# Performance work log

Measured on AMD Instinct MI355X. Metric: run time of the kernel, lower is better.

The kernel has to match this reference:

```python
import jax, jax.numpy as jnp
import numpy as np

# dims
H = 1024          # hidden_size
E = 2048          # d_inner = 2*H
NH = 32           # nheads = E/64
P = 64            # headdim
N = 128           # d_state
G = 1             # ngroups
K = 4             # d_conv
Q = 128           # SSD chunk length
FF = 4096         # intermediate_size
EPS = 1e-6        # rms_norm_eps
NEPS = 1e-5       # mamba gated-norm eps
CONV_DIM = E + 2 * G * N            # 2304
D_IN = 2 * E + 2 * G * N + NH       # 4384


def rmsnorm(x, w, eps):
    v = jnp.mean(x.astype(jnp.float32) ** 2, axis=-1, keepdims=True)
    return (x.astype(jnp.float32) * jax.lax.rsqrt(v + eps)).astype(x.dtype) * w


def segsum(x):
    # x: [..., T] -> [..., T, T] with out[i,j] = sum_{j<k<=i} x[k], -inf above diag
    T = x.shape[-1]
    cs = jnp.cumsum(x, axis=-1)
    s = cs[..., :, None] - cs[..., None, :]
    mask = jnp.tril(jnp.ones((T, T), dtype=bool))
    return jnp.where(mask, s, -jnp.inf)


def ssd(x, dt, A_log, B, C):
    # x:[b,l,nh,p], dt:[b,l,nh], B,C:[b,l,N] (ngroups=1, shared over heads)
    b, l, nh, p = x.shape
    A = -jnp.exp(A_log)                      # [nh]
    dA = dt * A                              # [b,l,nh]
    xd = x * dt[..., None]                   # discretized input
    c = l // Q
    xd = xd.reshape(b, c, Q, nh, p)
    dAc = dA.reshape(b, c, Q, nh).transpose(0, 3, 1, 2)   # [b,h,c,q]
    Bc = B.reshape(b, c, Q, N)
    Cc = C.reshape(b, c, Q, N)
    A_cs = jnp.cumsum(dAc, axis=-1)                        # [b,h,c,q]
    Lm = jnp.exp(segsum(dAc))                              # [b,h,c,q,q]
    # intra-chunk (diagonal blocks)
    Y_diag = jnp.einsum('bcqn,bcsn,bhcqs,bcshp->bcqhp', Cc, Bc, Lm, xd)
    # per-chunk final states
    decay_states = jnp.exp(A_cs[..., -1:] - A_cs)          # [b,h,c,q]
    states = jnp.einsum('bcqn,bhcq,bcqhp->bchpn', Bc, decay_states, xd)
    # inter-chunk recurrence (initial state = 0)
    A_last = jnp.pad(A_cs[..., -1], ((0, 0), (0, 0), (1, 0)))   # [b,h,c+1]
    decay_chunk = jnp.exp(segsum(A_last))                       # [b,h,c+1,c+1]
    states = jnp.concatenate([jnp.zeros_like(states[:, :1]), states], axis=1)
    new_states = jnp.einsum('bhzc,bchpn->bzhpn', decay_chunk, states)[:, :-1]
    Y_off = jnp.einsum('bcqn,bchpn,bhcq->bcqhp', Cc, new_states, jnp.exp(A_cs))
    return (Y_diag + Y_off).reshape(b, l, nh, p)


def mamba2(h, w_in, w_conv, b_conv, dt_bias, A_log, D, w_mnorm, w_out):
    b, l, _ = h.shape
    zxbcdt = h @ w_in.T                         # [b,l,D_IN]
    z, xBC, dt = jnp.split(zxbcdt, [E, E + CONV_DIM], axis=-1)
    # causal depthwise conv (kernel K) over channels of xBC
    pad = jnp.pad(xBC, ((0, 0), (K - 1, 0), (0, 0)))
    xBC = sum(pad[:, k:k + l, :] * w_conv[:, k] for k in range(K)) + b_conv
    xBC = jax.nn.silu(xBC)
    x, B, C = jnp.split(xBC, [E, E + G * N], axis=-1)
    dt = jax.nn.softplus(dt + dt_bias)          # [b,l,NH]
    xh = x.reshape(b, l, NH, P)
    y = ssd(xh, dt, A_log, B, C)
    y = y + D[None, None, :, None] * xh         # per-head skip
    y = y.reshape(b, l, E)
    y = rmsnorm(y * jax.nn.silu(z), w_mnorm, NEPS)   # gated RMSNorm
    return y @ w_out.T


def setup_inputs() -> dict:
    key = jax.random.key(0)
    ks = jax.random.split(key, 12)
    dt0 = jax.random.uniform(ks[0], (NH,), minval=0.001, maxval=0.1)
    dt_bias = dt0 + jnp.log(-jnp.expm1(-dt0))   # inverse softplus
    return {
        'hidden_states': jax.random.normal(ks[1], (2, 2048, H), dtype=jnp.float32),
        'w_ln1': jnp.ones((H,), jnp.float32),
        'w_in': 0.02 * jax.random.normal(ks[2], (D_IN, H), dtype=jnp.float32),
        'w_conv': 0.1 * jax.random.normal(ks[3], (CONV_DIM, K), dtype=jnp.float32),
        'b_conv': jnp.zeros((CONV_DIM,), jnp.float32),
        'dt_bias': dt_bias,
        'A_log': jnp.log(jax.random.uniform(ks[4], (NH,), minval=1.0, maxval=16.0)),
        'D': jnp.ones((NH,), jnp.float32),
        'w_mnorm': jnp.ones((E,), jnp.float32),
        'w_out': 0.02 * jax.random.normal(ks[5], (H, E), dtype=jnp.float32),
        'w_ln2': jnp.ones((H,), jnp.float32),
        'w_gate': 0.02 * jax.random.normal(ks[6], (FF, H), dtype=jnp.float32),
        'w_up': 0.02 * jax.random.normal(ks[7], (FF, H), dtype=jnp.float32),
        'w_down': 0.02 * jax.random.normal(ks[8], (H, FF), dtype=jnp.float32),
    }


def reference(hidden_states, w_ln1, w_in, w_conv, b_conv, dt_bias, A_log, D,
              w_mnorm, w_out, w_ln2, w_gate, w_up, w_down):
    residual = hidden_states
    h = rmsnorm(hidden_states, w_ln1, EPS)
    h = mamba2(h, w_in, w_conv, b_conv, dt_bias, A_log, D, w_mnorm, w_out)
    hidden = residual + h
    residual = hidden
    h = rmsnorm(hidden, w_ln2, EPS)
    h = (jax.nn.silu(h @ w_gate.T) * (h @ w_up.T)) @ w_down.T
    return residual + h
```

## Files before the change

### kernel.cpp

```cpp
#include <hip/hip_runtime.h>

#define DEV static __device__ __forceinline__

typedef short bf16x8 __attribute__((ext_vector_type(8)));
typedef float floatx4 __attribute__((ext_vector_type(4)));
typedef unsigned short ushort4v __attribute__((ext_vector_type(4)));
typedef unsigned short ushort8v __attribute__((ext_vector_type(8)));

DEV unsigned short f32_bf16(float f) {
  unsigned int u = __builtin_bit_cast(unsigned int, f);
  u = u + 0x7fffu + ((u >> 16) & 1u);
  return (unsigned short)(u >> 16);
}
DEV float bf2f(unsigned short u) {
  unsigned int v = ((unsigned int)u) << 16;
  return __builtin_bit_cast(float, v);
}
DEV float sigmoidf_(float x) { return 1.0f / (1.0f + __expf(-x)); }
DEV float siluf_(float x) { return x * sigmoidf_(x); }

#define GLD_LDS16(g, l)                                                              \
  __builtin_amdgcn_global_load_lds((const __attribute__((address_space(1))) void*)(g), \
                                   (__attribute__((address_space(3))) void*)(l), 16, 0, 0)

template <int MODE>
__global__ __launch_bounds__(256) void gemm128(
    const unsigned short* __restrict__ A, const unsigned short* __restrict__ B,
    void* __restrict__ Cv, const unsigned short* __restrict__ other,
    int K, int lda, int ldb, int ldc, long long bsA, long long bsB, long long bsC) {
  __shared__ unsigned short As[2 * 128 * 32];
  __shared__ unsigned short Bs[2 * 128 * 32];
  A += (long long)blockIdx.z * bsA;
  B += (long long)blockIdx.z * bsB;
  const long long coff = (long long)blockIdx.z * bsC;
  const int tid = threadIdx.x;
  const int w = tid >> 6, lane = tid & 63;

  const int nbx = gridDim.x, nby = gridDim.y;
  const int GM = 4;
  int bid = blockIdx.y * nbx + blockIdx.x;
  int gid = bid / (GM * nbx);
  int rem = bid - gid * (GM * nbx);
  int gsz = min(GM, nby - gid * GM);
  int mtile = gid * GM + rem % gsz;
  int ntile = rem / gsz;
  const int m0 = mtile << 7, n0 = ntile << 7;

  const int srow = lane >> 2;
  const int schunk = ((lane & 3) ^ (srow & 3)) * 8;
  const unsigned short* ag0 = A + (long long)(m0 + w * 32 + srow) * lda + schunk;
  const unsigned short* ag1 = ag0 + (long long)16 * lda;
  const unsigned short* bg0 = B + (long long)(n0 + w * 32 + srow) * ldb + schunk;
  const unsigned short* bg1 = bg0 + (long long)16 * ldb;
  const int s_off = w * 1024 + lane * 8;

#define STAGE128(buf, k0)                              \
  do {                                                 \
    GLD_LDS16(ag0 + (k0), As + (buf) * 4096 + s_off);  \
    GLD_LDS16(ag1 + (k0), As + (buf) * 4096 + s_off + 512); \
    GLD_LDS16(bg0 + (k0), Bs + (buf) * 4096 + s_off);  \
    GLD_LDS16(bg1 + (k0), Bs + (buf) * 4096 + s_off + 512); \
  } while (0)

  const int wr = (w >> 1) << 6, wc = (w & 1) << 6;
  const int fr = lane & 15;
  const int slot = (((lane >> 4) ^ (fr & 3))) << 3;

  floatx4 acc[4][4];
#pragma unroll
  for (int i = 0; i < 4; ++i)
#pragma unroll
    for (int j = 0; j < 4; ++j) acc[i][j] = (floatx4){0.f, 0.f, 0.f, 0.f};

  const int nsteps = K >> 5;
  STAGE128(0, 0);
  if (nsteps > 1) STAGE128(1, 32);

  for (int t = 0; t < nsteps; ++t) {
    if (t < nsteps - 1) {
      asm volatile("s_waitcnt vmcnt(4)" ::: "memory");
    } else {
      asm volatile("s_waitcnt vmcnt(0)" ::: "memory");
    }
    __builtin_amdgcn_s_barrier();
    __builtin_amdgcn_sched_barrier(0);
    const unsigned short* Ab = As + (t & 1) * 4096;
    const unsigned short* Bb = Bs + (t & 1) * 4096;
    bf16x8 af[4], bf_[4];
#pragma unroll
    for (int i = 0; i < 4; ++i)
      af[i] = *(const bf16x8*)(Ab + (wr + i * 16 + fr) * 32 + slot);
#pragma unroll
    for (int j = 0; j < 4; ++j)
      bf_[j] = *(const bf16x8*)(Bb + (wc + j * 16 + fr) * 32 + slot);
#pragma unroll
    for (int i = 0; i < 4; ++i)
#pragma unroll
      for (int j = 0; j < 4; ++j)
        acc[i][j] = __builtin_amdgcn_mfma_f32_16x16x32_bf16(af[i], bf_[j], acc[i][j], 0, 0, 0);
    __builtin_amdgcn_sched_barrier(0);
    __builtin_amdgcn_s_barrier();
    if (t + 2 < nsteps) STAGE128(t & 1, (t + 2) * 32);
  }
#undef STAGE128

  const int r0 = (lane >> 4) << 2;
#pragma unroll
  for (int i = 0; i < 4; ++i) {
#pragma unroll
    for (int j = 0; j < 4; ++j) {
      long long base = (long long)(m0 + wr + i * 16 + r0) * ldc + (n0 + wc + j * 16 + fr);
#pragma unroll
      for (int r = 0; r < 4; ++r) {
        long long idx = coff + base + (long long)r * ldc;
        float v = acc[i][j][r];
        if constexpr (MODE == 0) {
          ((float*)Cv)[idx] = v;
        } else if constexpr (MODE == 1) {
          ((unsigned short*)Cv)[idx] = f32_bf16(v);
        } else {
          ((unsigned short*)Cv)[idx] = f32_bf16(siluf_(v) * bf2f(other[idx]));
        }
      }
    }
  }
}

template <int WM>
__global__ __launch_bounds__(256) void gemm_small_nt(
    const unsigned short* __restrict__ A, const unsigned short* __restrict__ B,
    float* __restrict__ C, int M, int N, int K, int lda, int ldb, int ldc) {
  const int w = threadIdx.x >> 6;
  const int lane = threadIdx.x & 63;
  const int lm = lane & 15;
  const int ko = (lane >> 4) << 3;
  const int bn0 = blockIdx.x << 6;
  const int m_base = blockIdx.y * (WM * 64) + w * (WM * 16);

  const unsigned short* arow[WM];
#pragma unroll
  for (int i = 0; i < WM; ++i) arow[i] = A + (long long)(m_base + i * 16 + lm) * lda + ko;
  int nv = (N - bn0) >> 4;
  nv = nv > 4 ? 4 : nv;
  const unsigned short* brow[4];
#pragma unroll
  for (int j = 0; j < 4; ++j) {
    int nr = bn0 + j * 16 + lm;
    brow[j] = B + (long long)(j < nv ? nr : 0) * ldb + ko;
  }
  floatx4 acc[WM][4];
#pragma unroll
  for (int i = 0; i < WM; ++i)
#pragma unroll
    for (int j = 0; j < 4; ++j) acc[i][j] = (floatx4){0.f, 0.f, 0.f, 0.f};
  for (int k0 = 0; k0 < K; k0 += 32) {
    bf16x8 a[WM];
#pragma unroll
    for (int i = 0; i < WM; ++i) a[i] = *(const bf16x8*)(arow[i] + k0);
#pragma unroll
    for (int j = 0; j < 4; ++j) {
      if (j < nv) {
        bf16x8 b = *(const bf16x8*)(brow[j] + k0);
#pragma unroll
        for (int i = 0; i < WM; ++i)
          acc[i][j] = __builtin_amdgcn_mfma_f32_16x16x32_bf16(a[i], b, acc[i][j], 0, 0, 0);
      }
    }
  }
  const int r0 = (lane >> 4) << 2;
#pragma unroll
  for (int i = 0; i < WM; ++i)
#pragma unroll
    for (int j = 0; j < 4; ++j)
      if (j < nv) {
        int col = bn0 + j * 16 + lm;
        long long base = (long long)(m_base + i * 16 + r0) * ldc + col;
#pragma unroll
        for (int r = 0; r < 4; ++r) C[base + (long long)r * ldc] = acc[i][j][r];
      }
}

__global__ __launch_bounds__(256) void f32_to_bf16_k(const float* __restrict__ src,
                                                     unsigned short* __restrict__ dst,
                                                     long long n4) {
  long long i = (long long)blockIdx.x * 256 + threadIdx.x;
  if (i < n4) {
    float4 v = ((const float4*)src)[i];
    ushort4v o = {f32_bf16(v.x), f32_bf16(v.y), f32_bf16(v.z), f32_bf16(v.w)};
    ((ushort4v*)dst)[i] = o;
  }
}

__global__ __launch_bounds__(256) void zero_out_k(float* __restrict__ o, long long n) {
  long long i = (long long)blockIdx.x * 256 + threadIdx.x;
  if (i < n) o[i] = 0.f;
}

__global__ __launch_bounds__(256) void rmsnorm1024_bf16_k(const float* __restrict__ x,
                                                          const float* __restrict__ w,
                                                          unsigned short* __restrict__ out,
                                                          float eps) {
  long long row = blockIdx.x;
  int t = threadIdx.x;
  float4 v = ((const float4*)(x + row * 1024))[t];
  float ss = v.x * v.x + v.y * v.y + v.z * v.z + v.w * v.w;
  __shared__ float red[4];
#pragma unroll
  for (int o = 32; o > 0; o >>= 1) ss += __shfl_down(ss, o, 64);
  if ((t & 63) == 0) red[t >> 6] = ss;
  __syncthreads();
  float tot = red[0] + red[1] + red[2] + red[3];
  float sc = rsqrtf(tot * (1.0f / 1024.0f) + eps);
  float4 wv = ((const float4*)w)[t];
  ushort4v o = {f32_bf16(v.x * sc * wv.x), f32_bf16(v.y * sc * wv.y),
                f32_bf16(v.z * sc * wv.z), f32_bf16(v.w * sc * wv.w)};
  ((ushort4v*)(out + row * 1024))[t] = o;
}

__global__ __launch_bounds__(256) void add_rmsnorm_k(const float* __restrict__ hs,
                                                     const float* __restrict__ parts,
                                                     long long pstride, int np,
                                                     const float* __restrict__ w,
                                                     float* __restrict__ mh,
                                                     unsigned short* __restrict__ h2, float eps) {
  long long row = blockIdx.x;
  int t = threadIdx.x;
  float4 v = ((const float4*)(hs + row * 1024))[t];
  for (int p = 0; p < np; ++p) {
    float4 u = ((const float4*)(parts + p * pstride + row * 1024))[t];
    v.x += u.x;
    v.y += u.y;
    v.z += u.z;
    v.w += u.w;
  }
  ((float4*)(mh + row * 1024))[t] = v;
  float ss = v.x * v.x + v.y * v.y + v.z * v.z + v.w * v.w;
  __shared__ float red[4];
#pragma unroll
  for (int o = 32; o > 0; o >>= 1) ss += __shfl_down(ss, o, 64);
  if ((t & 63) == 0) red[t >> 6] = ss;
  __syncthreads();
  float tot = red[0] + red[1] + red[2] + red[3];
  float sc = rsqrtf(tot * (1.0f / 1024.0f) + eps);
  float4 wv = ((const float4*)w)[t];
  ushort4v o = {f32_bf16(v.x * sc * wv.x), f32_bf16(v.y * sc * wv.y),
                f32_bf16(v.z * sc * wv.z), f32_bf16(v.w * sc * wv.w)};
  ((ushort4v*)(h2 + row * 1024))[t] = o;
}

__global__ __launch_bounds__(256) void addn_f32_k(const float* __restrict__ a,
                                                  const float* __restrict__ parts,
                                                  long long pstride, int np,
                                                  float* __restrict__ o, long long n4) {
  long long i = (long long)blockIdx.x * 256 + threadIdx.x;
  if (i < n4) {
    float4 x = ((const float4*)a)[i];
    for (int p = 0; p < np; ++p) {
      float4 u = ((const float4*)(parts + p * pstride))[i];
      x.x += u.x;
      x.y += u.y;
      x.z += u.z;
      x.w += u.w;
    }
    ((float4*)o)[i] = x;
  }
}

__global__ __launch_bounds__(256) void gated_rmsnorm2048_k(const unsigned short* __restrict__ y,
                                                           const unsigned short* __restrict__ z,
                                                           const float* __restrict__ w,
                                                           unsigned short* __restrict__ out,
                                                           float eps) {
  long long row = blockIdx.x;
  int t = threadIdx.x;
  ushort8v yv = ((const ushort8v*)(y + row * 2048))[t];
  ushort8v zv = ((const ushort8v*)(z + row * 2048))[t];
  float g[8];
  float ss = 0.f;
#pragma unroll
  for (int j = 0; j < 8; ++j) {
    g[j] = bf2f(yv[j]) * siluf_(bf2f(zv[j]));
    ss += g[j] * g[j];
  }
  __shared__ float red[4];
#pragma unroll
  for (int o = 32; o > 0; o >>= 1) ss += __shfl_down(ss, o, 64);
  if ((t & 63) == 0) red[t >> 6] = ss;
  __syncthreads();
  float tot = red[0] + red[1] + red[2] + red[3];
  float sc = rsqrtf(tot * (1.0f / 2048.0f) + eps);
  float ww[8];
  *(float4*)&ww[0] = ((const float4*)w)[2 * t];
  *(float4*)&ww[4] = ((const float4*)w)[2 * t + 1];
  ushort8v o;
#pragma unroll
  for (int j = 0; j < 8; ++j) o[j] = f32_bf16(g[j] * sc * ww[j]);
  ((ushort8v*)(out + row * 2048))[t] = o;
}

__global__ __launch_bounds__(256) void conv_silu_k(const unsigned short* __restrict__ xraw,
                                                   const float* __restrict__ wconv,
                                                   const float* __restrict__ bconv,
                                                   unsigned short* __restrict__ xBC) {
  int m = blockIdx.x;
  int l = m & 2047;
  for (int cb = threadIdx.x; cb < 288; cb += 256) {
    int ch0 = cb << 3;
    float acc[8];
    float4 bc0 = ((const float4*)bconv)[cb * 2];
    float4 bc1 = ((const float4*)bconv)[cb * 2 + 1];
    acc[0] = bc0.x; acc[1] = bc0.y; acc[2] = bc0.z; acc[3] = bc0.w;
    acc[4] = bc1.x; acc[5] = bc1.y; acc[6] = bc1.z; acc[7] = bc1.w;
    float4 wv[8];
#pragma unroll
    for (int j = 0; j < 8; ++j) wv[j] = ((const float4*)wconv)[ch0 + j];
#pragma unroll
    for (int k = 0; k < 4; ++k) {
      int lk = l + k - 3;
      if (lk >= 0) {
        ushort8v xv = *(const ushort8v*)(xraw + (long long)(m + k - 3) * 2304 + ch0);
        acc[0] += bf2f(xv[0]) * ((const float*)&wv[0])[k];
        acc[1] += bf2f(xv[1]) * ((const float*)&wv[1])[k];
        acc[2] += bf2f(xv[2]) * ((const float*)&wv[2])[k];
        acc[3] += bf2f(xv[3]) * ((const float*)&wv[3])[k];
        acc[4] += bf2f(xv[4]) * ((const float*)&wv[4])[k];
        acc[5] += bf2f(xv[5]) * ((const float*)&wv[5])[k];
        acc[6] += bf2f(xv[6]) * ((const float*)&wv[6])[k];
        acc[7] += bf2f(xv[7]) * ((const float*)&wv[7])[k];
      }
    }
    ushort8v o;
#pragma unroll
    for (int j = 0; j < 8; ++j) o[j] = f32_bf16(siluf_(acc[j]));
    *(ushort8v*)(xBC + (long long)m * 2304 + ch0) = o;
  }
}

__global__ __launch_bounds__(256) void dt_softplus_k(const float* __restrict__ dtraw,
                                                     const float* __restrict__ dt_bias,
                                                     float* __restrict__ dt_s) {
  int i = blockIdx.x * 256 + threadIdx.x;
  float xv = dtraw[i] + dt_bias[i & 31];
  dt_s[i] = xv > 20.f ? xv : log1pf(expf(xv));
}

__global__ __launch_bounds__(128) void dA_cumsum_k(const float* __restrict__ dt_s,
                                                   const float* __restrict__ A_log,
                                                   float* __restrict__ dA_cs) {
  int bi = blockIdx.x;
  int c = bi & 15, h = (bi >> 4) & 31, b = bi >> 9;
  int q = threadIdx.x;
  float A = -expf(A_log[h]);
  float v = dt_s[((long long)(b * 2048 + c * 128 + q)) * 32 + h] * A;
  __shared__ float sbuf[128];
  sbuf[q] = v;
  __syncthreads();
  for (int off = 1; off < 128; off <<= 1) {
    float tv = (q >= off) ? sbuf[q - off] : 0.f;
    __syncthreads();
    sbuf[q] += tv;
    __syncthreads();
  }
  dA_cs[(long long)bi * 128 + q] = sbuf[q];
}

__global__ __launch_bounds__(256) void ssd_diag_states_k(
    const unsigned short* __restrict__ xBC, const float* __restrict__ dt_s,
    const float* __restrict__ dA_cs, const unsigned short* __restrict__ G,
    unsigned short* __restrict__ y, unsigned short* __restrict__ states) {
  __shared__ unsigned short Mz[128 * 136];
  __shared__ unsigned short xdT[64 * 136];
  __shared__ float Acs[128];
  __shared__ float wdec[128];
  const int bx = blockIdx.x;
  const int h = bx & 31, c = (bx >> 5) & 15, b = bx >> 9;
  const int t = threadIdx.x;
  const int w = t >> 6, lane = t & 63, fr = lane & 15, hi = lane >> 4;
  const long long rowbase = (long long)b * 2048 + c * 128;
  const long long abase = ((long long)((b * 32 + h) * 16 + c)) << 7;

  if (t < 128) {
    float a = dA_cs[abase + t];
    Acs[t] = a;
    wdec[t] = __expf(dA_cs[abase + 127] - a);
  }
  {
    int s = t >> 1, p0 = (t & 1) * 32;
    float dtv = dt_s[(rowbase + s) * 32 + h];
    const ushort8v* xv = (const ushort8v*)(xBC + (rowbase + s) * 2304 + h * 64 + p0);
#pragma unroll
    for (int i = 0; i < 4; ++i) {
      ushort8v vv = xv[i];
#pragma unroll
      for (int j = 0; j < 8; ++j) xdT[(p0 + i * 8 + j) * 136 + s] = f32_bf16(bf2f(vv[j]) * dtv);
    }
  }
  __syncthreads();
  {
    int q = t >> 1, s0 = (t & 1) * 64;
    float aq = Acs[q];
    const ushort8v* gv =
        (const ushort8v*)(G + (((long long)(b * 16 + c)) * 128 + q) * 128 + s0);
#pragma unroll
    for (int i = 0; i < 8; ++i) {
      ushort8v gg = gv[i];
#pragma unroll
      for (int j = 0; j < 8; ++j) {
        int s = s0 + i * 8 + j;
        float m = (s <= q) ? bf2f(gg[j]) * __expf(aq - Acs[s]) : 0.f;
        Mz[q * 136 + s] = f32_bf16(m);
      }
    }
  }
  __syncthreads();
  const int q0 = w << 5;
  {
    floatx4 acc[2][4];
#pragma unroll
    for (int i = 0; i < 2; ++i)
#pragma unroll
      for (int j = 0; j < 4; ++j) acc[i][j] = (floatx4){0.f, 0.f, 0.f, 0.f};
#pragma unroll
    for (int k0 = 0; k0 < 128; k0 += 32) {
      int kk = k0 + hi * 8;
      bf16x8 a0 = *(const bf16x8*)(Mz + (q0 + fr) * 136 + kk);
      bf16x8 a1 = *(const bf16x8*)(Mz + (q0 + 16 + fr) * 136 + kk);
      bf16x8 bf_[4];
#pragma unroll
      for (int j = 0; j < 4; ++j) bf_[j] = *(const bf16x8*)(xdT + (j * 16 + fr) * 136 + kk);
#pragma unroll
      for (int j = 0; j < 4; ++j) {
        acc[0][j] = __builtin_amdgcn_mfma_f32_16x16x32_bf16(a0, bf_[j], acc[0][j], 0, 0, 0);
        acc[1][j] = __builtin_amdgcn_mfma_f32_16x16x32_bf16(a1, bf_[j], acc[1][j], 0, 0, 0);
      }
    }
#pragma unroll
    for (int i = 0; i < 2; ++i)
#pragma unroll
      for (int r = 0; r < 4; ++r) {
        int q = q0 + i * 16 + hi * 4 + r;
        unsigned short* yrow = y + (rowbase + q) * 2048 + h * 64;
#pragma unroll
        for (int j = 0; j < 4; ++j) yrow[j * 16 + fr] = f32_bf16(acc[i][j][r]);
      }
  }
  __syncthreads();
  {
    int s = t >> 1, n0 = (t & 1) * 64;
    float wd = wdec[s];
    const ushort8v* bv = (const ushort8v*)(xBC + (rowbase + s) * 2304 + 2048 + n0);
#pragma unroll
    for (int i = 0; i < 8; ++i) {
      ushort8v bb = bv[i];
#pragma unroll
      for (int j = 0; j < 8; ++j) Mz[(n0 + i * 8 + j) * 136 + s] = f32_bf16(bf2f(bb[j]) * wd);
    }
  }
  __syncthreads();
  {
    floatx4 acc[2][4];
#pragma unroll
    for (int i = 0; i < 2; ++i)
#pragma unroll
      for (int j = 0; j < 4; ++j) acc[i][j] = (floatx4){0.f, 0.f, 0.f, 0.f};
#pragma unroll
    for (int k0 = 0; k0 < 128; k0 += 32) {
      int kk = k0 + hi * 8;
      bf16x8 a0 = *(const bf16x8*)(Mz + (q0 + fr) * 136 + kk);
      bf16x8 a1 = *(const bf16x8*)(Mz + (q0 + 16 + fr) * 136 + kk);
      bf16x8 bf_[4];
#pragma unroll
      for (int j = 0; j < 4; ++j) bf_[j] = *(const bf16x8*)(xdT + (j * 16 + fr) * 136 + kk);
#pragma unroll
      for (int j = 0; j < 4; ++j) {
        acc[0][j] = __builtin_amdgcn_mfma_f32_16x16x32_bf16(a0, bf_[j], acc[0][j], 0, 0, 0);
        acc[1][j] = __builtin_amdgcn_mfma_f32_16x16x32_bf16(a1, bf_[j], acc[1][j], 0, 0, 0);
      }
    }
    unsigned short* st = states + (long long)bx * 8192;
#pragma unroll
    for (int i = 0; i < 2; ++i)
#pragma unroll
      for (int j = 0; j < 4; ++j) {
        int p = j * 16 + fr;
        int n = q0 + i * 16 + hi * 4;
        ushort4v o;
#pragma unroll
        for (int r = 0; r < 4; ++r) o[r] = f32_bf16(acc[i][j][r]);
        *(ushort4v*)(st + p * 128 + n) = o;
      }
  }
}

__global__ __launch_bounds__(256) void ssd_scan_k(const float* __restrict__ dA_cs,
                                                  unsigned short* __restrict__ states) {
  int seg = blockIdx.x & 7;
  int h = (blockIdx.x >> 3) & 31;
  int b = blockIdx.x >> 8;
  int t = threadIdx.x;
  int e0 = seg * 1024 + t;
  float carry[4];
#pragma unroll
  for (int i = 0; i < 4; ++i) carry[i] = 0.f;
  for (int c = 0; c < 16; ++c) {
    long long base = ((long long)((b * 16 + c) * 32 + h)) * 8192;
    float dec = __expf(dA_cs[(((long long)((b * 32 + h) * 16 + c)) << 7) + 127]);
#pragma unroll
    for (int i = 0; i < 4; ++i) {
      long long idx = base + e0 + i * 256;
      float local = bf2f(states[idx]);
      states[idx] = f32_bf16(carry[i]);
      carry[i] = dec * carry[i] + local;
    }
  }
}

__global__ __launch_bounds__(256) void ssd_off_k(const unsigned short* __restrict__ xBC,
                                                 const float* __restrict__ dA_cs,
                                                 const unsigned short* __restrict__ states,
                                                 const float* __restrict__ Dvec,
                                                 unsigned short* __restrict__ y) {
  __shared__ float eA[128];
  const int bx = blockIdx.x;
  const int h = bx & 31, c = (bx >> 5) & 15, b = bx >> 9;
  const int t = threadIdx.x;
  const int w = t >> 6, lane = t & 63, fr = lane & 15, hi = lane >> 4;
  const long long rowbase = (long long)b * 2048 + c * 128;
  const long long abase = ((long long)((b * 32 + h) * 16 + c)) << 7;
  if (t < 128) eA[t] = __expf(dA_cs[abase + t]);
  __syncthreads();

  const unsigned short* st = states + (long long)bx * 8192;
  const int q0 = w << 5;
  floatx4 acc[2][4];
#pragma unroll
  for (int i = 0; i < 2; ++i)
#pragma unroll
    for (int j = 0; j < 4; ++j) acc[i][j] = (floatx4){0.f, 0.f, 0.f, 0.f};

#pragma unroll
  for (int k0 = 0; k0 < 128; k0 += 32) {
    int kk = k0 + hi * 8;
    bf16x8 a0 = *(const bf16x8*)(xBC + (rowbase + q0 + fr) * 2304 + 2176 + kk);
    bf16x8 a1 = *(const bf16x8*)(xBC + (rowbase + q0 + 16 + fr) * 2304 + 2176 + kk);
    bf16x8 bf_[4];
#pragma unroll
    for (int j = 0; j < 4; ++j) bf_[j] = *(const bf16x8*)(st + (j * 16 + fr) * 128 + kk);
#pragma unroll
    for (int j = 0; j < 4; ++j) {
      acc[0][j] = __builtin_amdgcn_mfma_f32_16x16x32_bf16(a0, bf_[j], acc[0][j], 0, 0, 0);
      acc[1][j] = __builtin_amdgcn_mfma_f32_16x16x32_bf16(a1, bf_[j], acc[1][j], 0, 0, 0);
    }
  }

  float Dh = Dvec[h];
#pragma unroll
  for (int i = 0; i < 2; ++i) {
#pragma unroll
    for (int r = 0; r < 4; ++r) {
      int q = q0 + i * 16 + hi * 4 + r;
      float e = eA[q];
      const unsigned short* xrow = xBC + (rowbase + q) * 2304 + h * 64;
      unsigned short* yrow = y + (rowbase + q) * 2048 + h * 64;
#pragma unroll
      for (int j = 0; j < 4; ++j) {
        int p = j * 16 + fr;
        float v = bf2f(yrow[p]) + e * acc[i][j][r] + Dh * bf2f(xrow[p]);
        yrow[p] = f32_bf16(v);
      }
    }
  }
}

extern "C" void kernel_launch(void* const* d_in, const int* in_sizes, int n_in, void* d_out,
                              int out_size, void* d_ws, size_t ws_size, hipStream_t stream) {
  const float* hs = (const float*)d_in[0];
  const float* w_ln1 = (const float*)d_in[1];
  const float* w_in = (const float*)d_in[2];
  const float* w_conv = (const float*)d_in[3];
  const float* b_conv = (const float*)d_in[4];
  const float* dt_bias = (const float*)d_in[5];
  const float* A_log = (const float*)d_in[6];
  const float* Dvec = (const float*)d_in[7];
  const float* w_mnorm = (const float*)d_in[8];
  const float* w_out = (const float*)d_in[9];
  const float* w_ln2 = (const float*)d_in[10];
  const float* w_gate = (const float*)d_in[11];
  const float* w_up = (const float*)d_in[12];
  const float* w_down = (const float*)d_in[13];
  float* out = (float*)d_out;
  const int M = 4096;

  char* ws = (char*)d_ws;
  const size_t R0 = 0;
  const size_t R1 = 33554432;
  const size_t R1b = R1 + 33554432;
  const size_t R2 = 71303168;
  const size_t R3 = 90177536;
  const size_t R4 = 107544576;
  const size_t W0 = 108068864;
  const size_t NEED = 133234688;

  if (ws_size < NEED) {
    hipLaunchKernelGGL(zero_out_k, dim3((out_size + 255) / 256), dim3(256), 0, stream, out,
                       (long long)out_size);
    return;
  }

  unsigned short* z = (unsigned short*)(ws + R0);
  unsigned short* act = (unsigned short*)(ws + R0);
  float* oproj_parts = (float*)(ws + R0);
  unsigned short* xraw = (unsigned short*)(ws + R1);
  unsigned short* states = (unsigned short*)(ws + R1);
  unsigned short* ybuf = (unsigned short*)(ws + R1 + 16777216);
  unsigned short* upo = (unsigned short*)(ws + R1);
  float* down_parts = (float*)(ws + R1);
  unsigned short* wbf_out = (unsigned short*)(ws + R1b);
  unsigned short* xBC = (unsigned short*)(ws + R2);
  unsigned short* ygn = (unsigned short*)(ws + R2);
  unsigned short* h2 = (unsigned short*)(ws + R2);
  unsigned short* hnorm = (unsigned short*)(ws + R3);
  unsigned short* wbf_in = (unsigned short*)(ws + R3 + 8388608);
  float* dt_s = (float*)(ws + R3);
  float* dA_cs = (float*)(ws + R3 + 524288);
  unsigned short* Gbuf = (unsigned short*)(ws + R3 + 1048576);
  float* mh = (float*)(ws + R3);
  float* dtraw = (float*)(ws + R4);
  unsigned short* wbf_gate = (unsigned short*)(ws + W0);
  unsigned short* wbf_up = (unsigned short*)(ws + W0 + 8388608);
  unsigned short* wbf_down = (unsigned short*)(ws + W0 + 16777216);

  hipLaunchKernelGGL(rmsnorm1024_bf16_k, dim3(M), dim3(256), 0, stream, hs, w_ln1, hnorm, 1e-6f);
  hipLaunchKernelGGL(f32_to_bf16_k, dim3(4384), dim3(256), 0, stream, w_in, wbf_in, 1122304LL);
  hipLaunchKernelGGL(f32_to_bf16_k, dim3(4096), dim3(256), 0, stream, w_gate, wbf_gate, 1048576LL);
  hipLaunchKernelGGL(f32_to_bf16_k, dim3(4096), dim3(256), 0, stream, w_up, wbf_up, 1048576LL);
  hipLaunchKernelGGL(f32_to_bf16_k, dim3(4096), dim3(256), 0, stream, w_down, wbf_down, 1048576LL);
  hipLaunchKernelGGL((gemm128<1>), dim3(16, 32, 1), dim3(256), 0, stream, hnorm, wbf_in, (void*)z,
                     (const unsigned short*)nullptr, 1024, 1024, 1024, 2048, 0LL, 0LL, 0LL);
  hipLaunchKernelGGL((gemm128<1>), dim3(18, 32, 1), dim3(256), 0, stream, hnorm,
                     wbf_in + 2048 * 1024, (void*)xraw, (const unsigned short*)nullptr, 1024, 1024,
                     1024, 2304, 0LL, 0LL, 0LL);
  hipLaunchKernelGGL((gemm_small_nt<4>), dim3(1, 16, 1), dim3(256), 0, stream, hnorm,
                     wbf_in + 4352 * 1024, dtraw, M, 32, 1024, 1024, 1024, 32);
  hipLaunchKernelGGL(conv_silu_k, dim3(M), dim3(256), 0, stream, xraw, w_conv, b_conv, xBC);
  hipLaunchKernelGGL(f32_to_bf16_k, dim3(2048), dim3(256), 0, stream, w_out, wbf_out, 524288LL);
  hipLaunchKernelGGL(dt_softplus_k, dim3(512), dim3(256), 0, stream, dtraw, dt_bias, dt_s);
  hipLaunchKernelGGL(dA_cumsum_k, dim3(1024), dim3(128), 0, stream, dt_s, A_log, dA_cs);
  hipLaunchKernelGGL((gemm128<1>), dim3(1, 1, 32), dim3(256), 0, stream, xBC + 2176, xBC + 2048,
                     (void*)Gbuf, (const unsigned short*)nullptr, 128, 2304, 2304, 128, 294912LL,
                     294912LL, 16384LL);
  hipLaunchKernelGGL(ssd_diag_states_k, dim3(1024), dim3(256), 0, stream, xBC, dt_s, dA_cs, Gbuf,
                     ybuf, states);
  hipLaunchKernelGGL(ssd_scan_k, dim3(512), dim3(256), 0, stream, dA_cs, states);
  hipLaunchKernelGGL(ssd_off_k, dim3(1024), dim3(256), 0, stream, xBC, dA_cs, states, Dvec, ybuf);
  hipLaunchKernelGGL(gated_rmsnorm2048_k, dim3(M), dim3(256), 0, stream, ybuf, z, w_mnorm, ygn,
                     1e-5f);
  hipLaunchKernelGGL((gemm128<0>), dim3(8, 32, 4), dim3(256), 0, stream, ygn, wbf_out,
                     (void*)oproj_parts, (const unsigned short*)nullptr, 512, 2048, 2048, 1024,
                     512LL, 512LL, 4194304LL);
  hipLaunchKernelGGL(add_rmsnorm_k, dim3(M), dim3(256), 0, stream, hs, oproj_parts, 4194304LL, 4,
                     w_ln2, mh, h2, 1e-6f);
  hipLaunchKernelGGL((gemm128<1>), dim3(32, 32, 1), dim3(256), 0, stream, h2, wbf_up, (void*)upo,
                     (const unsigned short*)nullptr, 1024, 1024, 1024, 4096, 0LL, 0LL, 0LL);
  hipLaunchKernelGGL((gemm128<2>), dim3(32, 32, 1), dim3(256), 0, stream, h2, wbf_gate, (void*)act,
                     upo, 1024, 1024, 1024, 4096, 0LL, 0LL, 0LL);
  hipLaunchKernelGGL((gemm128<0>), dim3(8, 32, 2), dim3(256), 0, stream, act, wbf_down,
                     (void*)down_parts, (const unsigned short*)nullptr, 2048, 4096, 4096, 1024,
                     2048LL, 2048LL, 4194304LL);
  hipLaunchKernelGGL(addn_f32_k, dim3(4096), dim3(256), 0, stream, mh, down_parts, 4194304LL, 2,
                     out, 1048576LL);
}
```

Before: 573.5 us.

## Triple-buffer GEMM LDS stages and vectorize bf16 epilogue through shared memory

The main 128x128 GEMM kernel moves from double to triple buffering in LDS. The next-next stage is issued right after the top barrier, which removes the second per-iteration barrier and lets global loads overlap the MFMA work. For the bf16 output modes, accumulators are staged through LDS in two passes so each thread writes 16-byte vectorized rows instead of scattered 2-byte stores. The fused silu*up epilogue also reads the other operand as 8-wide vectors. LDS use grows to 48KB, which may reduce occupancy.

```diff
diff --git a/kernel.cpp b/kernel.cpp
--- a/kernel.cpp
+++ b/kernel.cpp
@@ -28,8 +28,7 @@
     const unsigned short* __restrict__ A, const unsigned short* __restrict__ B,
     void* __restrict__ Cv, const unsigned short* __restrict__ other,
     int K, int lda, int ldb, int ldc, long long bsA, long long bsB, long long bsC) {
-  __shared__ unsigned short As[2 * 128 * 32];
-  __shared__ unsigned short Bs[2 * 128 * 32];
+  __shared__ unsigned short S[3 * 8192];
   A += (long long)blockIdx.z * bsA;
   B += (long long)blockIdx.z * bsB;
   const long long coff = (long long)blockIdx.z * bsC;
@@ -54,17 +53,20 @@
   const unsigned short* bg1 = bg0 + (long long)16 * ldb;
   const int s_off = w * 1024 + lane * 8;
 
-#define STAGE128(buf, k0)                              \
-  do {                                                 \
-    GLD_LDS16(ag0 + (k0), As + (buf) * 4096 + s_off);  \
-    GLD_LDS16(ag1 + (k0), As + (buf) * 4096 + s_off + 512); \
-    GLD_LDS16(bg0 + (k0), Bs + (buf) * 4096 + s_off);  \
-    GLD_LDS16(bg1 + (k0), Bs + (buf) * 4096 + s_off + 512); \
+#define STAGE128(buf, k0)                               \
+  do {                                                  \
+    unsigned short* as_ = S + (buf) * 8192;             \
+    unsigned short* bs_ = as_ + 4096;                   \
+    GLD_LDS16(ag0 + (k0), as_ + s_off);                 \
+    GLD_LDS16(ag1 + (k0), as_ + s_off + 512);           \
+    GLD_LDS16(bg0 + (k0), bs_ + s_off);                 \
+    GLD_LDS16(bg1 + (k0), bs_ + s_off + 512);           \
   } while (0)
 
   const int wr = (w >> 1) << 6, wc = (w & 1) << 6;
   const int fr = lane & 15;
   const int slot = (((lane >> 4) ^ (fr & 3))) << 3;
+  const int r0 = (lane >> 4) << 2;
 
   floatx4 acc[4][4];
 #pragma unroll
@@ -76,6 +78,7 @@
   STAGE128(0, 0);
   if (nsteps > 1) STAGE128(1, 32);
 
+  int cur = 0, nxt2 = 2;
   for (int t = 0; t < nsteps; ++t) {
     if (t < nsteps - 1) {
       asm volatile("s_waitcnt vmcnt(4)" ::: "memory");
@@ -84,8 +87,10 @@
     }
     __builtin_amdgcn_s_barrier();
     __builtin_amdgcn_sched_barrier(0);
-    const unsigned short* Ab = As + (t & 1) * 4096;
-    const unsigned short* Bb = Bs + (t & 1) * 4096;
+    if (t + 2 < nsteps) STAGE128(nxt2, (t + 2) * 32);
+    __builtin_amdgcn_sched_barrier(0);
+    const unsigned short* Ab = S + cur * 8192;
+    const unsigned short* Bb = Ab + 4096;
     bf16x8 af[4], bf_[4];
 #pragma unroll
     for (int i = 0; i < 4; ++i)
@@ -99,29 +104,63 @@
       for (int j = 0; j < 4; ++j)
         acc[i][j] = __builtin_amdgcn_mfma_f32_16x16x32_bf16(af[i], bf_[j], acc[i][j], 0, 0, 0);
     __builtin_amdgcn_sched_barrier(0);
-    __builtin_amdgcn_s_barrier();
-    if (t + 2 < nsteps) STAGE128(t & 1, (t + 2) * 32);
+    cur = (cur == 2) ? 0 : cur + 1;
+    nxt2 = (nxt2 == 2) ? 0 : nxt2 + 1;
   }
 #undef STAGE128
 
-  const int r0 = (lane >> 4) << 2;
-#pragma unroll
-  for (int i = 0; i < 4; ++i) {
-#pragma unroll
-    for (int j = 0; j < 4; ++j) {
-      long long base = (long long)(m0 + wr + i * 16 + r0) * ldc + (n0 + wc + j * 16 + fr);
-#pragma unroll
-      for (int r = 0; r < 4; ++r) {
-        long long idx = coff + base + (long long)r * ldc;
-        float v = acc[i][j][r];
-        if constexpr (MODE == 0) {
-          ((float*)Cv)[idx] = v;
-        } else if constexpr (MODE == 1) {
-          ((unsigned short*)Cv)[idx] = f32_bf16(v);
+  if constexpr (MODE == 0) {
+#pragma unroll
+    for (int i = 0; i < 4; ++i) {
+#pragma unroll
+      for (int j = 0; j < 4; ++j) {
+        long long base = (long long)(m0 + wr + i * 16 + r0) * ldc + (n0 + wc + j * 16 + fr);
+#pragma unroll
+        for (int r = 0; r < 4; ++r) {
+          ((float*)Cv)[coff + base + (long long)r * ldc] = acc[i][j][r];
+        }
+      }
+    }
+  } else {
+    float* scr = (float*)S;
+    const int row_l = tid >> 2;
+    const int c0 = (tid & 3) << 5;
+    __syncthreads();
+#pragma unroll
+    for (int pass = 0; pass < 2; ++pass) {
+      if ((w >> 1) == pass) {
+#pragma unroll
+        for (int i = 0; i < 4; ++i) {
+#pragma unroll
+          for (int j = 0; j < 4; ++j) {
+            int rl = i * 16 + r0;
+            int col = wc + j * 16 + fr;
+#pragma unroll
+            for (int r = 0; r < 4; ++r) scr[(rl + r) * 132 + col] = acc[i][j][r];
+          }
+        }
+      }
+      __syncthreads();
+      long long grow = m0 + pass * 64 + row_l;
+      long long gbase = coff + grow * ldc + (n0 + c0);
+      const float* srow_p = scr + row_l * 132 + c0;
+#pragma unroll
+      for (int k = 0; k < 4; ++k) {
+        float v[8];
+        *(float4*)&v[0] = *(const float4*)(srow_p + k * 8);
+        *(float4*)&v[4] = *(const float4*)(srow_p + k * 8 + 4);
+        ushort8v o;
+        if constexpr (MODE == 2) {
+          ushort8v uo = *(const ushort8v*)(other + gbase + k * 8);
+#pragma unroll
+          for (int e = 0; e < 8; ++e) o[e] = f32_bf16(siluf_(v[e]) * bf2f(uo[e]));
         } else {
-          ((unsigned short*)Cv)[idx] = f32_bf16(siluf_(v) * bf2f(other[idx]));
+#pragma unroll
+          for (int e = 0; e < 8; ++e) o[e] = f32_bf16(v[e]);
         }
-      }
+        *(ushort8v*)((unsigned short*)Cv + gbase + k * 8) = o;
+      }
+      __syncthreads();
     }
   }
 }
```

Result: faster. 560.4 us (-2.3%).
